# Optimization experiments

Hardware: AMD Instinct MI355X
Metric: run time of the kernel (lower is better)

## Reference

```python
import jax, jax.numpy as jnp
import numpy as np

B, N, E = 32, 2000, 32000      # graphs, nodes/graph, edges/graph
V, D, R, K = 100000, 128, 39, 8  # vocab, emb_dim, n_relation, n_bases
EPS = 1e-5


def setup_inputs() -> dict:
    key = jax.random.key(0)
    ks = jax.random.split(key, 8)
    node_ids = jax.random.randint(ks[0], (B, N), 0, V)
    edge_index = jax.random.randint(ks[1], (B, 2, E), 0, N)
    edge_type = jax.random.randint(ks[2], (B, E), 0, R)
    embedding = jax.random.normal(ks[3], (V, D), jnp.float32) * D ** -0.5
    bases = jax.random.normal(ks[4], (K, D, D), jnp.float32) * D ** -0.5
    comp = jax.random.normal(ks[5], (R, K), jnp.float32) * K ** -0.5
    root = jax.random.normal(ks[6], (D, D), jnp.float32) * D ** -0.5
    bias = jnp.zeros((D,), jnp.float32)
    return dict(node_ids=node_ids, edge_index=edge_index, edge_type=edge_type,
                embedding=embedding, bases=bases, comp=comp, root=root, bias=bias)


def _graph_fwd(node_ids, edge_index, edge_type, embedding, bases, comp, root, bias):
    # RGCNConv with basis decomposition and per-relation MEAN aggregation (PyG default).
    x = embedding[node_ids]                       # [N, D] per-graph node features
    src, dst = edge_index[0], edge_index[1]       # j -> i, aggregate at dst
    x_src = x[src]                                # [E, D]
    # mean normalizer per (dst, relation) bucket
    comb = dst * R + edge_type                    # [E]
    cnt = jax.ops.segment_sum(jnp.ones((E,), jnp.float32), comb, num_segments=N * R)
    inv = jnp.where(cnt > 0, 1.0 / cnt, 0.0)[comb]  # [E]
    # W_r = sum_k comp[r,k] * bases[k]; fold comp coefficients + mean norm into edge weights
    w = comp[edge_type] * inv[:, None]            # [E, K]
    out = x @ root + bias                         # root/self connection
    for k in range(K):                            # small fixed loop over bases
        zk = jax.ops.segment_sum(w[:, k:k + 1] * x_src, dst, num_segments=N)  # [N, D]
        out = out + zk @ bases[k]
    g = out.sum(axis=0)                           # sum pool over nodes
    # torch.nn.functional.normalize(p=2, eps=1e-5)
    return g / jnp.maximum(jnp.linalg.norm(g), EPS)


def reference(node_ids, edge_index, edge_type, embedding, bases, comp, root, bias):
    f = jax.vmap(_graph_fwd, in_axes=(0, 0, 0, None, None, None, None, None))
    return f(node_ids, edge_index, edge_type, embedding, bases, comp, root, bias)  # [B, D]
```

## Files before the change

kernel.cpp:

```cpp
#include <hip/hip_runtime.h>
#include <math.h>

#define Bn 32
#define Nn 2000
#define En 32000
#define Vn 100000
#define Dn 128
#define Rn 39
#define Kn 8

#define SUBS 8
#define NPS (Nn / SUBS)
#define CH 128
#define EQ (En / 4)


__global__ __launch_bounds__(1024) void cnt_kernel(const int* __restrict__ edge_index,
                                                   const int* __restrict__ edge_type,
                                                   int* __restrict__ cnt) {
    int b = blockIdx.x, sub = blockIdx.y;
    int s0 = sub * NPS;
    __shared__ int loc[NPS * Rn];
    for (int i = threadIdx.x; i < NPS * Rn; i += 1024) loc[i] = 0;
    __syncthreads();
    const int4* dst4 = (const int4*)(edge_index + (b * 2 + 1) * En);
    const int4* et4  = (const int4*)(edge_type + b * En);
    for (int q = threadIdx.x; q < EQ; q += 1024) {
        int4 d = dst4[q];
        int4 t = et4[q];
        int x;
        x = d.x - s0; if ((unsigned)x < NPS) atomicAdd(&loc[x * Rn + t.x], 1);
        x = d.y - s0; if ((unsigned)x < NPS) atomicAdd(&loc[x * Rn + t.y], 1);
        x = d.z - s0; if ((unsigned)x < NPS) atomicAdd(&loc[x * Rn + t.z], 1);
        x = d.w - s0; if ((unsigned)x < NPS) atomicAdd(&loc[x * Rn + t.w], 1);
    }
    __syncthreads();
    int* g = cnt + ((size_t)b * Nn + s0) * Rn;
    for (int i = threadIdx.x; i < NPS * Rn; i += 1024) g[i] = loc[i];
}

__global__ __launch_bounds__(256) void inv_kernel(const int* __restrict__ edge_index,
                                                  const int* __restrict__ edge_type,
                                                  const int* __restrict__ cnt,
                                                  float* __restrict__ inv) {
    int b = blockIdx.x;
    int q = blockIdx.y * 256 + threadIdx.x;
    if (q >= EQ) return;
    int4 d = ((const int4*)(edge_index + (b * 2 + 1) * En))[q];
    int4 t = ((const int4*)(edge_type + b * En))[q];
    const int* cb = cnt + (size_t)b * Nn * Rn;
    float4 r;
    r.x = 1.0f / (float)cb[d.x * Rn + t.x];
    r.y = 1.0f / (float)cb[d.y * Rn + t.y];
    r.z = 1.0f / (float)cb[d.z * Rn + t.z];
    r.w = 1.0f / (float)cb[d.w * Rn + t.w];
    ((float4*)(inv + (size_t)b * En))[q] = r;
}

__global__ __launch_bounds__(1024) void a_kernel(const int* __restrict__ edge_index,
                                                 const int* __restrict__ edge_type,
                                                 const float* __restrict__ inv,
                                                 const float* __restrict__ comp,
                                                 float* __restrict__ a) {
    int b = blockIdx.x, sub = blockIdx.y;
    int s0 = sub * NPS;
    __shared__ float s[NPS * Rn];
    __shared__ float comp_l[Rn * Kn];
    for (int i = threadIdx.x; i < NPS * Rn; i += 1024) s[i] = 0.0f;
    if (threadIdx.x < Rn * Kn) comp_l[threadIdx.x] = comp[threadIdx.x];
    __syncthreads();
    const int4*   src4 = (const int4*)(edge_index + (b * 2 + 0) * En);
    const int4*   et4  = (const int4*)(edge_type + b * En);
    const float4* iv4  = (const float4*)(inv + (size_t)b * En);
    for (int q = threadIdx.x; q < EQ; q += 1024) {
        int4 sv = src4[q];
        int4 tv = et4[q];
        float4 iv = iv4[q];
        int x;
        x = sv.x - s0; if ((unsigned)x < NPS) atomicAdd(&s[x * Rn + tv.x], iv.x);
        x = sv.y - s0; if ((unsigned)x < NPS) atomicAdd(&s[x * Rn + tv.y], iv.y);
        x = sv.z - s0; if ((unsigned)x < NPS) atomicAdd(&s[x * Rn + tv.z], iv.z);
        x = sv.w - s0; if ((unsigned)x < NPS) atomicAdd(&s[x * Rn + tv.w], iv.w);
    }
    __syncthreads();
    float* g = a + ((size_t)b * Nn + s0) * Kn;
    for (int i = threadIdx.x; i < NPS * Kn; i += 1024) {
        int n = i >> 3, k = i & 7;
        float acc = 0.0f;
        const float* srow = &s[n * Rn];
        for (int t = 0; t < Rn; t++) acc += srow[t] * comp_l[t * Kn + k];
        g[i] = acc;
    }
}

__global__ __launch_bounds__(256) void gather_kernel(const int* __restrict__ node_ids,
                                                     const float* __restrict__ emb,
                                                     const float* __restrict__ a,
                                                     float* __restrict__ partial) {
    int b = blockIdx.x, c = blockIdx.y;
    int lane = threadIdx.x & 63, wv = threadIdx.x >> 6;
    float acc[18];
#pragma unroll
    for (int k = 0; k < 18; k++) acc[k] = 0.0f;
    const int* nb = node_ids + b * Nn;
    for (int n = c * 4 + wv; n < Nn; n += 2 * CH * 4) {
        int n2 = n + CH * 4;
        bool has2 = n2 < Nn;
        int nid  = nb[n];
        int nid2 = has2 ? nb[n2] : 0;
        float2 v  = ((const float2*)(emb + (size_t)nid  * Dn))[lane];
        float2 v2 = has2 ? ((const float2*)(emb + (size_t)nid2 * Dn))[lane]
                         : make_float2(0.f, 0.f);
        const float4* ar = (const float4*)(a + ((size_t)b * Nn + n) * Kn);
        float4 a0 = ar[0], a1 = ar[1];
        float w[9] = {a0.x, a0.y, a0.z, a0.w, a1.x, a1.y, a1.z, a1.w, 1.0f};
#pragma unroll
        for (int k = 0; k < 9; k++) { acc[2*k] += w[k] * v.x; acc[2*k+1] += w[k] * v.y; }
        if (has2) {
            const float4* ar2 = (const float4*)(a + ((size_t)b * Nn + n2) * Kn);
            float4 b0 = ar2[0], b1 = ar2[1];
            float w2[9] = {b0.x, b0.y, b0.z, b0.w, b1.x, b1.y, b1.z, b1.w, 1.0f};
#pragma unroll
            for (int k = 0; k < 9; k++) { acc[2*k] += w2[k] * v2.x; acc[2*k+1] += w2[k] * v2.y; }
        }
    }
    __shared__ float red[4 * 9 * Dn];
#pragma unroll
    for (int k = 0; k < 9; k++) {
        ((float2*)&red[(wv * 9 + k) * Dn])[lane] = make_float2(acc[2*k], acc[2*k+1]);
    }
    __syncthreads();
    float* g = partial + ((size_t)b * CH + c) * 9 * Dn;
    for (int i = threadIdx.x; i < 9 * Dn; i += 256)
        g[i] = red[i] + red[9 * Dn + i] + red[18 * Dn + i] + red[27 * Dn + i];
}

__global__ __launch_bounds__(256) void matvec_kernel(const float* __restrict__ partial,
                                                     const float* __restrict__ root,
                                                     const float* __restrict__ bases,
                                                     float* __restrict__ gmat) {
    int b = blockIdx.x, m = blockIdx.y;
    int d = threadIdx.x & (Dn - 1), h = threadIdx.x >> 7;
    __shared__ float ts[Dn];
    __shared__ float tsh[2][Dn];
    const float* p = partial + (size_t)b * CH * 9 * Dn + m * Dn + d;
    float sum = 0.0f;
    for (int c = h; c < CH; c += 2) sum += p[(size_t)c * 9 * Dn];
    tsh[h][d] = sum;
    __syncthreads();
    if (h == 0) ts[d] = tsh[0][d] + tsh[1][d];
    __syncthreads();
    const float* M = (m == 8) ? root : bases + (size_t)m * Dn * Dn;
    float g = 0.0f;
    for (int j = h * 64; j < h * 64 + 64; j++) g += ts[j] * M[j * Dn + d];
    __syncthreads();
    tsh[h][d] = g;
    __syncthreads();
    if (h == 0) gmat[((size_t)b * 9 + m) * Dn + d] = tsh[0][d] + tsh[1][d];
}

__global__ __launch_bounds__(128) void norm_kernel(const float* __restrict__ gmat,
                                                   const float* __restrict__ bias,
                                                   float* __restrict__ out) {
    int b = blockIdx.x, d = threadIdx.x;
    float g = (float)Nn * bias[d];
    const float* gb = gmat + (size_t)b * 9 * Dn + d;
#pragma unroll
    for (int m = 0; m < 9; m++) g += gb[m * Dn];
    float ss = g * g;
#pragma unroll
    for (int off = 32; off > 0; off >>= 1) ss += __shfl_down(ss, off, 64);
    __shared__ float s2[2];
    if ((threadIdx.x & 63) == 0) s2[threadIdx.x >> 6] = ss;
    __syncthreads();
    float nrm = sqrtf(s2[0] + s2[1]);
    out[b * Dn + d] = g / fmaxf(nrm, 1e-5f);
}

extern "C" void kernel_launch(void* const* d_in, const int* in_sizes, int n_in,
                              void* d_out, int out_size, void* d_ws, size_t ws_size,
                              hipStream_t stream) {
    const int*   node_ids   = (const int*)d_in[0];
    const int*   edge_index = (const int*)d_in[1];
    const int*   edge_type  = (const int*)d_in[2];
    const float* embedding  = (const float*)d_in[3];
    const float* bases      = (const float*)d_in[4];
    const float* comp       = (const float*)d_in[5];
    const float* root       = (const float*)d_in[6];
    const float* bias       = (const float*)d_in[7];
    float*       out        = (float*)d_out;

    char* w = (char*)d_ws;
    int*   cnt     = (int*)  (w + 0);
    float* inv     = (float*)(w + 9984000);
    float* a       = (float*)(w + 14080000);
    float* partial = (float*)(w + 16128000);
    float* gmat    = (float*)(w + 35004416);

    cnt_kernel   <<<dim3(Bn, SUBS), 1024, 0, stream>>>(edge_index, edge_type, cnt);
    inv_kernel   <<<dim3(Bn, (EQ + 255) / 256), 256, 0, stream>>>(edge_index, edge_type, cnt, inv);
    a_kernel     <<<dim3(Bn, SUBS), 1024, 0, stream>>>(edge_index, edge_type, inv, comp, a);
    gather_kernel<<<dim3(Bn, CH),   256,  0, stream>>>(node_ids, embedding, a, partial);
    matvec_kernel<<<dim3(Bn, 9),    256,  0, stream>>>(partial, root, bases, gmat);
    norm_kernel  <<<Bn, 128, 0, stream>>>(gmat, bias, out);
}
```

Measured before the change: 166.7 us.

## Fuse inverse-count into a_kernel and merge matvec with normalization kernel

Computes the per-edge mean normalizer inline in a_kernel by reading the count table directly, removing the inv kernel and its buffer. Merges chunk reduction, the nine basis/root matvecs and the L2 normalization into a single per-graph kernel. Reduces gather chunks and unrolls four node loads per wave for more memory-level parallelism. Removes two launches and intermediate traffic, but the final kernel now runs only one block per graph serially over all nine matrices.

Result: slower. 254.7 us (+52.8%).

```diff
diff --git a/kernel.cpp b/kernel.cpp
--- a/kernel.cpp
+++ b/kernel.cpp
@@ -11,7 +11,7 @@
 
 #define SUBS 8
 #define NPS (Nn / SUBS)
-#define CH 128
+#define CH 32
 #define EQ (En / 4)
 
 
@@ -39,27 +39,9 @@
     for (int i = threadIdx.x; i < NPS * Rn; i += 1024) g[i] = loc[i];
 }
 
-__global__ __launch_bounds__(256) void inv_kernel(const int* __restrict__ edge_index,
-                                                  const int* __restrict__ edge_type,
-                                                  const int* __restrict__ cnt,
-                                                  float* __restrict__ inv) {
-    int b = blockIdx.x;
-    int q = blockIdx.y * 256 + threadIdx.x;
-    if (q >= EQ) return;
-    int4 d = ((const int4*)(edge_index + (b * 2 + 1) * En))[q];
-    int4 t = ((const int4*)(edge_type + b * En))[q];
-    const int* cb = cnt + (size_t)b * Nn * Rn;
-    float4 r;
-    r.x = 1.0f / (float)cb[d.x * Rn + t.x];
-    r.y = 1.0f / (float)cb[d.y * Rn + t.y];
-    r.z = 1.0f / (float)cb[d.z * Rn + t.z];
-    r.w = 1.0f / (float)cb[d.w * Rn + t.w];
-    ((float4*)(inv + (size_t)b * En))[q] = r;
-}
-
 __global__ __launch_bounds__(1024) void a_kernel(const int* __restrict__ edge_index,
                                                  const int* __restrict__ edge_type,
-                                                 const float* __restrict__ inv,
+                                                 const int* __restrict__ cnt,
                                                  const float* __restrict__ comp,
                                                  float* __restrict__ a) {
     int b = blockIdx.x, sub = blockIdx.y;
@@ -69,18 +51,23 @@
     for (int i = threadIdx.x; i < NPS * Rn; i += 1024) s[i] = 0.0f;
     if (threadIdx.x < Rn * Kn) comp_l[threadIdx.x] = comp[threadIdx.x];
     __syncthreads();
-    const int4*   src4 = (const int4*)(edge_index + (b * 2 + 0) * En);
-    const int4*   et4  = (const int4*)(edge_type + b * En);
-    const float4* iv4  = (const float4*)(inv + (size_t)b * En);
+    const int4* src4 = (const int4*)(edge_index + (b * 2 + 0) * En);
+    const int4* dst4 = (const int4*)(edge_index + (b * 2 + 1) * En);
+    const int4* et4  = (const int4*)(edge_type + b * En);
+    const int*  cb   = cnt + (size_t)b * Nn * Rn;
     for (int q = threadIdx.x; q < EQ; q += 1024) {
         int4 sv = src4[q];
+        int4 dv = dst4[q];
         int4 tv = et4[q];
-        float4 iv = iv4[q];
         int x;
-        x = sv.x - s0; if ((unsigned)x < NPS) atomicAdd(&s[x * Rn + tv.x], iv.x);
-        x = sv.y - s0; if ((unsigned)x < NPS) atomicAdd(&s[x * Rn + tv.y], iv.y);
-        x = sv.z - s0; if ((unsigned)x < NPS) atomicAdd(&s[x * Rn + tv.z], iv.z);
-        x = sv.w - s0; if ((unsigned)x < NPS) atomicAdd(&s[x * Rn + tv.w], iv.w);
+        x = sv.x - s0; if ((unsigned)x < NPS)
+            atomicAdd(&s[x * Rn + tv.x], 1.0f / (float)cb[dv.x * Rn + tv.x]);
+        x = sv.y - s0; if ((unsigned)x < NPS)
+            atomicAdd(&s[x * Rn + tv.y], 1.0f / (float)cb[dv.y * Rn + tv.y]);
+        x = sv.z - s0; if ((unsigned)x < NPS)
+            atomicAdd(&s[x * Rn + tv.z], 1.0f / (float)cb[dv.z * Rn + tv.z]);
+        x = sv.w - s0; if ((unsigned)x < NPS)
+            atomicAdd(&s[x * Rn + tv.w], 1.0f / (float)cb[dv.w * Rn + tv.w]);
     }
     __syncthreads();
     float* g = a + ((size_t)b * Nn + s0) * Kn;
@@ -99,35 +86,46 @@
                                                      float* __restrict__ partial) {
     int b = blockIdx.x, c = blockIdx.y;
     int lane = threadIdx.x & 63, wv = threadIdx.x >> 6;
+    int W = c * 4 + wv;
     float acc[18];
 #pragma unroll
     for (int k = 0; k < 18; k++) acc[k] = 0.0f;
-    const int* nb = node_ids + b * Nn;
-    for (int n = c * 4 + wv; n < Nn; n += 2 * CH * 4) {
-        int n2 = n + CH * 4;
-        bool has2 = n2 < Nn;
-        int nid  = nb[n];
-        int nid2 = has2 ? nb[n2] : 0;
-        float2 v  = ((const float2*)(emb + (size_t)nid  * Dn))[lane];
-        float2 v2 = has2 ? ((const float2*)(emb + (size_t)nid2 * Dn))[lane]
-                         : make_float2(0.f, 0.f);
-        const float4* ar = (const float4*)(a + ((size_t)b * Nn + n) * Kn);
-        float4 a0 = ar[0], a1 = ar[1];
-        float w[9] = {a0.x, a0.y, a0.z, a0.w, a1.x, a1.y, a1.z, a1.w, 1.0f};
+    const int*   nb = node_ids + b * Nn;
+    const float* ab = a + (size_t)b * Nn * Kn;
+    for (int n0 = W; n0 < Nn; n0 += 4 * 128) {
+        bool  has[4];
+        int   nn[4];
+        float2 v[4];
+        float4 a0[4], a1[4];
 #pragma unroll
-        for (int k = 0; k < 9; k++) { acc[2*k] += w[k] * v.x; acc[2*k+1] += w[k] * v.y; }
-        if (has2) {
-            const float4* ar2 = (const float4*)(a + ((size_t)b * Nn + n2) * Kn);
-            float4 b0 = ar2[0], b1 = ar2[1];
-            float w2[9] = {b0.x, b0.y, b0.z, b0.w, b1.x, b1.y, b1.z, b1.w, 1.0f};
+        for (int i = 0; i < 4; i++) {
+            int n = n0 + i * 128;
+            has[i] = n < Nn;
+            nn[i]  = has[i] ? n : n0;
+        }
 #pragma unroll
-            for (int k = 0; k < 9; k++) { acc[2*k] += w2[k] * v2.x; acc[2*k+1] += w2[k] * v2.y; }
+        for (int i = 0; i < 4; i++) {
+            int nid = nb[nn[i]];
+            v[i] = has[i] ? ((const float2*)(emb + (size_t)nid * Dn))[lane]
+                          : make_float2(0.f, 0.f);
+            const float4* ar = (const float4*)(ab + (size_t)nn[i] * Kn);
+            a0[i] = ar[0]; a1[i] = ar[1];
+        }
+#pragma unroll
+        for (int i = 0; i < 4; i++) {
+            float w[9] = {a0[i].x, a0[i].y, a0[i].z, a0[i].w,
+                          a1[i].x, a1[i].y, a1[i].z, a1[i].w, 1.0f};
+#pragma unroll
+            for (int k = 0; k < 9; k++) {
+                acc[2 * k]     += w[k] * v[i].x;
+                acc[2 * k + 1] += w[k] * v[i].y;
+            }
         }
     }
     __shared__ float red[4 * 9 * Dn];
 #pragma unroll
     for (int k = 0; k < 9; k++) {
-        ((float2*)&red[(wv * 9 + k) * Dn])[lane] = make_float2(acc[2*k], acc[2*k+1]);
+        ((float2*)&red[(wv * 9 + k) * Dn])[lane] = make_float2(acc[2 * k], acc[2 * k + 1]);
     }
     __syncthreads();
     float* g = partial + ((size_t)b * CH + c) * 9 * Dn;
@@ -135,46 +133,41 @@
         g[i] = red[i] + red[9 * Dn + i] + red[18 * Dn + i] + red[27 * Dn + i];
 }
 
-__global__ __launch_bounds__(256) void matvec_kernel(const float* __restrict__ partial,
-                                                     const float* __restrict__ root,
-                                                     const float* __restrict__ bases,
-                                                     float* __restrict__ gmat) {
-    int b = blockIdx.x, m = blockIdx.y;
+__global__ __launch_bounds__(256) void final_kernel(const float* __restrict__ partial,
+                                                    const float* __restrict__ root,
+                                                    const float* __restrict__ bases,
+                                                    const float* __restrict__ bias,
+                                                    float* __restrict__ out) {
+    int b = blockIdx.x;
+    __shared__ float ts[9 * Dn];
+    for (int i = threadIdx.x; i < 9 * Dn; i += 256) {
+        float s = 0.0f;
+        const float* p = partial + (size_t)b * CH * 9 * Dn + i;
+        for (int c = 0; c < CH; c++) s += p[c * 9 * Dn];
+        ts[i] = s;
+    }
+    __syncthreads();
     int d = threadIdx.x & (Dn - 1), h = threadIdx.x >> 7;
-    __shared__ float ts[Dn];
-    __shared__ float tsh[2][Dn];
-    const float* p = partial + (size_t)b * CH * 9 * Dn + m * Dn + d;
-    float sum = 0.0f;
-    for (int c = h; c < CH; c += 2) sum += p[(size_t)c * 9 * Dn];
-    tsh[h][d] = sum;
+    float gp = 0.0f;
+#pragma unroll
+    for (int m = 0; m < 9; m++) {
+        const float* M  = (m == 8) ? root : bases + (size_t)m * Dn * Dn;
+        const float* tm = &ts[m * Dn];
+        for (int j = h * 64; j < h * 64 + 64; j++) gp += tm[j] * M[j * Dn + d];
+    }
+    __shared__ float gsh[2][Dn];
+    gsh[h][d] = gp;
     __syncthreads();
-    if (h == 0) ts[d] = tsh[0][d] + tsh[1][d];
-    __syncthreads();
-    const float* M = (m == 8) ? root : bases + (size_t)m * Dn * Dn;
     float g = 0.0f;
-    for (int j = h * 64; j < h * 64 + 64; j++) g += ts[j] * M[j * Dn + d];
-    __syncthreads();
-    tsh[h][d] = g;
-    __syncthreads();
-    if (h == 0) gmat[((size_t)b * 9 + m) * Dn + d] = tsh[0][d] + tsh[1][d];
-}
-
-__global__ __launch_bounds__(128) void norm_kernel(const float* __restrict__ gmat,
-                                                   const float* __restrict__ bias,
-                                                   float* __restrict__ out) {
-    int b = blockIdx.x, d = threadIdx.x;
-    float g = (float)Nn * bias[d];
-    const float* gb = gmat + (size_t)b * 9 * Dn + d;
-#pragma unroll
-    for (int m = 0; m < 9; m++) g += gb[m * Dn];
+    if (h == 0) g = (float)Nn * bias[d] + gsh[0][d] + gsh[1][d];
     float ss = g * g;
 #pragma unroll
     for (int off = 32; off > 0; off >>= 1) ss += __shfl_down(ss, off, 64);
-    __shared__ float s2[2];
-    if ((threadIdx.x & 63) == 0) s2[threadIdx.x >> 6] = ss;
+    __shared__ float s4[4];
+    if ((threadIdx.x & 63) == 0) s4[threadIdx.x >> 6] = ss;
     __syncthreads();
-    float nrm = sqrtf(s2[0] + s2[1]);
-    out[b * Dn + d] = g / fmaxf(nrm, 1e-5f);
+    float nrm = sqrtf(s4[0] + s4[1] + s4[2] + s4[3]);
+    if (h == 0) out[b * Dn + d] = g / fmaxf(nrm, 1e-5f);
 }
 
 extern "C" void kernel_launch(void* const* d_in, const int* in_sizes, int n_in,
@@ -192,15 +185,11 @@
 
     char* w = (char*)d_ws;
     int*   cnt     = (int*)  (w + 0);
-    float* inv     = (float*)(w + 9984000);
-    float* a       = (float*)(w + 14080000);
-    float* partial = (float*)(w + 16128000);
-    float* gmat    = (float*)(w + 35004416);
+    float* a       = (float*)(w + 9984000);
+    float* partial = (float*)(w + 12032000);
 
     cnt_kernel   <<<dim3(Bn, SUBS), 1024, 0, stream>>>(edge_index, edge_type, cnt);
-    inv_kernel   <<<dim3(Bn, (EQ + 255) / 256), 256, 0, stream>>>(edge_index, edge_type, cnt, inv);
-    a_kernel     <<<dim3(Bn, SUBS), 1024, 0, stream>>>(edge_index, edge_type, inv, comp, a);
+    a_kernel     <<<dim3(Bn, SUBS), 1024, 0, stream>>>(edge_index, edge_type, cnt, comp, a);
     gather_kernel<<<dim3(Bn, CH),   256,  0, stream>>>(node_ids, embedding, a, partial);
-    matvec_kernel<<<dim3(Bn, 9),    256,  0, stream>>>(partial, root, bases, gmat);
-    norm_kernel  <<<Bn, 128, 0, stream>>>(gmat, bias, out);
+    final_kernel <<<Bn, 256, 0, stream>>>(partial, root, bases, bias, out);
 }
```

## Fuse count and inverse kernels; restructure gather to per-wave partials

Applied to the files above, without the earlier changes.

Merges the per-bucket count and inverse-normalizer kernels so each block computes its inverse weights straight from its shared-memory counts. This drops the global count buffer and one launch. The gather kernel now has each wave write its own partial, with four nodes of loads in flight per iteration, instead of reducing through shared memory. It also launches fewer blocks (32 per graph). The matvec reduction is unrolled with four accumulators. The trade-offs are lower gather occupancy and a rescan of the edge list in the fused kernel.

Result: faster. 156.1 us, median of 2 (-6.3%).

```diff
diff --git a/kernel.cpp b/kernel.cpp
--- a/kernel.cpp
+++ b/kernel.cpp
@@ -11,13 +11,13 @@
 
 #define SUBS 8
 #define NPS (Nn / SUBS)
-#define CH 128
+#define WPG 128
 #define EQ (En / 4)
 
 
-__global__ __launch_bounds__(1024) void cnt_kernel(const int* __restrict__ edge_index,
-                                                   const int* __restrict__ edge_type,
-                                                   int* __restrict__ cnt) {
+__global__ __launch_bounds__(1024) void cntinv_kernel(const int* __restrict__ edge_index,
+                                                      const int* __restrict__ edge_type,
+                                                      float* __restrict__ inv) {
     int b = blockIdx.x, sub = blockIdx.y;
     int s0 = sub * NPS;
     __shared__ int loc[NPS * Rn];
@@ -35,26 +35,16 @@
         x = d.w - s0; if ((unsigned)x < NPS) atomicAdd(&loc[x * Rn + t.w], 1);
     }
     __syncthreads();
-    int* g = cnt + ((size_t)b * Nn + s0) * Rn;
-    for (int i = threadIdx.x; i < NPS * Rn; i += 1024) g[i] = loc[i];
-}
-
-__global__ __launch_bounds__(256) void inv_kernel(const int* __restrict__ edge_index,
-                                                  const int* __restrict__ edge_type,
-                                                  const int* __restrict__ cnt,
-                                                  float* __restrict__ inv) {
-    int b = blockIdx.x;
-    int q = blockIdx.y * 256 + threadIdx.x;
-    if (q >= EQ) return;
-    int4 d = ((const int4*)(edge_index + (b * 2 + 1) * En))[q];
-    int4 t = ((const int4*)(edge_type + b * En))[q];
-    const int* cb = cnt + (size_t)b * Nn * Rn;
-    float4 r;
-    r.x = 1.0f / (float)cb[d.x * Rn + t.x];
-    r.y = 1.0f / (float)cb[d.y * Rn + t.y];
-    r.z = 1.0f / (float)cb[d.z * Rn + t.z];
-    r.w = 1.0f / (float)cb[d.w * Rn + t.w];
-    ((float4*)(inv + (size_t)b * En))[q] = r;
+    float* ivb = inv + (size_t)b * En;
+    for (int q = threadIdx.x; q < EQ; q += 1024) {
+        int4 d = dst4[q];
+        int4 t = et4[q];
+        int e = 4 * q, x;
+        x = d.x - s0; if ((unsigned)x < NPS) ivb[e]     = 1.0f / (float)loc[x * Rn + t.x];
+        x = d.y - s0; if ((unsigned)x < NPS) ivb[e + 1] = 1.0f / (float)loc[x * Rn + t.y];
+        x = d.z - s0; if ((unsigned)x < NPS) ivb[e + 2] = 1.0f / (float)loc[x * Rn + t.z];
+        x = d.w - s0; if ((unsigned)x < NPS) ivb[e + 3] = 1.0f / (float)loc[x * Rn + t.w];
+    }
 }
 
 __global__ __launch_bounds__(1024) void a_kernel(const int* __restrict__ edge_index,
@@ -97,42 +87,48 @@
                                                      const float* __restrict__ emb,
                                                      const float* __restrict__ a,
                                                      float* __restrict__ partial) {
-    int b = blockIdx.x, c = blockIdx.y;
+    int b = blockIdx.x;
     int lane = threadIdx.x & 63, wv = threadIdx.x >> 6;
+    int W = blockIdx.y * 4 + wv;
     float acc[18];
 #pragma unroll
     for (int k = 0; k < 18; k++) acc[k] = 0.0f;
-    const int* nb = node_ids + b * Nn;
-    for (int n = c * 4 + wv; n < Nn; n += 2 * CH * 4) {
-        int n2 = n + CH * 4;
-        bool has2 = n2 < Nn;
-        int nid  = nb[n];
-        int nid2 = has2 ? nb[n2] : 0;
-        float2 v  = ((const float2*)(emb + (size_t)nid  * Dn))[lane];
-        float2 v2 = has2 ? ((const float2*)(emb + (size_t)nid2 * Dn))[lane]
-                         : make_float2(0.f, 0.f);
-        const float4* ar = (const float4*)(a + ((size_t)b * Nn + n) * Kn);
-        float4 a0 = ar[0], a1 = ar[1];
-        float w[9] = {a0.x, a0.y, a0.z, a0.w, a1.x, a1.y, a1.z, a1.w, 1.0f};
-#pragma unroll
-        for (int k = 0; k < 9; k++) { acc[2*k] += w[k] * v.x; acc[2*k+1] += w[k] * v.y; }
-        if (has2) {
-            const float4* ar2 = (const float4*)(a + ((size_t)b * Nn + n2) * Kn);
-            float4 b0 = ar2[0], b1 = ar2[1];
-            float w2[9] = {b0.x, b0.y, b0.z, b0.w, b1.x, b1.y, b1.z, b1.w, 1.0f};
-#pragma unroll
-            for (int k = 0; k < 9; k++) { acc[2*k] += w2[k] * v2.x; acc[2*k+1] += w2[k] * v2.y; }
+    const int*   nb = node_ids + b * Nn;
+    const float* ab = a + (size_t)b * Nn * Kn;
+    for (int n0 = W; n0 < Nn; n0 += 4 * WPG) {
+        bool   has[4];
+        int    nn[4];
+        float2 v[4];
+        float4 a0[4], a1[4];
+#pragma unroll
+        for (int i = 0; i < 4; i++) {
+            int n = n0 + i * WPG;
+            has[i] = n < Nn;
+            nn[i]  = has[i] ? n : n0;
         }
-    }
-    __shared__ float red[4 * 9 * Dn];
-#pragma unroll
-    for (int k = 0; k < 9; k++) {
-        ((float2*)&red[(wv * 9 + k) * Dn])[lane] = make_float2(acc[2*k], acc[2*k+1]);
-    }
-    __syncthreads();
-    float* g = partial + ((size_t)b * CH + c) * 9 * Dn;
-    for (int i = threadIdx.x; i < 9 * Dn; i += 256)
-        g[i] = red[i] + red[9 * Dn + i] + red[18 * Dn + i] + red[27 * Dn + i];
+#pragma unroll
+        for (int i = 0; i < 4; i++) {
+            int nid = nb[nn[i]];
+            v[i] = has[i] ? ((const float2*)(emb + (size_t)nid * Dn))[lane]
+                          : make_float2(0.f, 0.f);
+            const float4* ar = (const float4*)(ab + (size_t)nn[i] * Kn);
+            a0[i] = ar[0]; a1[i] = ar[1];
+        }
+#pragma unroll
+        for (int i = 0; i < 4; i++) {
+            float w[9] = {a0[i].x, a0[i].y, a0[i].z, a0[i].w,
+                          a1[i].x, a1[i].y, a1[i].z, a1[i].w, 1.0f};
+#pragma unroll
+            for (int k = 0; k < 9; k++) {
+                acc[2 * k]     += w[k] * v[i].x;
+                acc[2 * k + 1] += w[k] * v[i].y;
+            }
+        }
+    }
+    float2* gp = (float2*)(partial + ((size_t)b * WPG + W) * 9 * Dn);
+#pragma unroll
+    for (int k = 0; k < 9; k++)
+        gp[k * 64 + lane] = make_float2(acc[2 * k], acc[2 * k + 1]);
 }
 
 __global__ __launch_bounds__(256) void matvec_kernel(const float* __restrict__ partial,
@@ -143,10 +139,15 @@
     int d = threadIdx.x & (Dn - 1), h = threadIdx.x >> 7;
     __shared__ float ts[Dn];
     __shared__ float tsh[2][Dn];
-    const float* p = partial + (size_t)b * CH * 9 * Dn + m * Dn + d;
-    float sum = 0.0f;
-    for (int c = h; c < CH; c += 2) sum += p[(size_t)c * 9 * Dn];
-    tsh[h][d] = sum;
+    const float* p = partial + (size_t)b * WPG * 9 * Dn + m * Dn + d;
+    float s0 = 0.f, s1 = 0.f, s2 = 0.f, s3 = 0.f;
+    for (int c = h; c < WPG; c += 8) {
+        s0 += p[(size_t)(c    ) * 9 * Dn];
+        s1 += p[(size_t)(c + 2) * 9 * Dn];
+        s2 += p[(size_t)(c + 4) * 9 * Dn];
+        s3 += p[(size_t)(c + 6) * 9 * Dn];
+    }
+    tsh[h][d] = (s0 + s1) + (s2 + s3);
     __syncthreads();
     if (h == 0) ts[d] = tsh[0][d] + tsh[1][d];
     __syncthreads();
@@ -191,16 +192,14 @@
     float*       out        = (float*)d_out;
 
     char* w = (char*)d_ws;
-    int*   cnt     = (int*)  (w + 0);
-    float* inv     = (float*)(w + 9984000);
-    float* a       = (float*)(w + 14080000);
-    float* partial = (float*)(w + 16128000);
-    float* gmat    = (float*)(w + 35004416);
-
-    cnt_kernel   <<<dim3(Bn, SUBS), 1024, 0, stream>>>(edge_index, edge_type, cnt);
-    inv_kernel   <<<dim3(Bn, (EQ + 255) / 256), 256, 0, stream>>>(edge_index, edge_type, cnt, inv);
-    a_kernel     <<<dim3(Bn, SUBS), 1024, 0, stream>>>(edge_index, edge_type, inv, comp, a);
-    gather_kernel<<<dim3(Bn, CH),   256,  0, stream>>>(node_ids, embedding, a, partial);
-    matvec_kernel<<<dim3(Bn, 9),    256,  0, stream>>>(partial, root, bases, gmat);
+    float* inv     = (float*)(w + 0);
+    float* a       = (float*)(w + 4096000);
+    float* partial = (float*)(w + 6144000);
+    float* gmat    = (float*)(w + 25018368);
+
+    cntinv_kernel<<<dim3(Bn, SUBS),    1024, 0, stream>>>(edge_index, edge_type, inv);
+    a_kernel     <<<dim3(Bn, SUBS),    1024, 0, stream>>>(edge_index, edge_type, inv, comp, a);
+    gather_kernel<<<dim3(Bn, WPG / 4), 256,  0, stream>>>(node_ids, embedding, a, partial);
+    matvec_kernel<<<dim3(Bn, 9),       256,  0, stream>>>(partial, root, bases, gmat);
     norm_kernel  <<<Bn, 128, 0, stream>>>(gmat, bias, out);
 }
```
